# Kernel tuning notes

Measured on AMD Instinct MI355X. Metric: run time of the kernel, lower is better.

Reference implementation:

```python
import jax, jax.numpy as jnp
import numpy as np

NUM_NODES = 50000
NUM_RELS = 47        # 2*23 + 1 after enrich()
EMB_DIM = 1600
WEIGHTS_SIZE = 16
NUM_CLASSES = 50
BASES = 40
NUM_EDGES = 1600000


def setup_inputs() -> dict:
    key = jax.random.key(0)
    ks = jax.random.split(key, 8)
    return {
        "node_embeddings": jax.random.normal(ks[0], (NUM_NODES, EMB_DIM), jnp.float32),
        "comps1": jax.random.normal(ks[1], (NUM_RELS, BASES), jnp.float32),
        "bases1": jax.random.normal(ks[2], (BASES, EMB_DIM, WEIGHTS_SIZE), jnp.float32) * 0.05,
        "comps2": jax.random.normal(ks[3], (NUM_RELS, BASES), jnp.float32),
        "bases2": jax.random.normal(ks[4], (BASES, WEIGHTS_SIZE, NUM_CLASSES), jnp.float32) * 0.05,
        "bias1": jnp.zeros((WEIGHTS_SIZE,), jnp.float32),
        "bias2": jnp.zeros((NUM_CLASSES,), jnp.float32),
        "rows": jax.random.randint(ks[5], (NUM_EDGES,), 0, NUM_NODES, jnp.int32),
        "cols": jax.random.randint(ks[6], (NUM_EDGES,), 0, NUM_RELS * NUM_NODES, jnp.int32),
    }


def _spmm(rows, cols, vals, h_rel):
    # hor_graph @ h_rel : h_rel is (R*N, d); out[n] = sum_e vals[e] * h_rel[cols[e]]
    msgs = vals[:, None] * h_rel[cols]              # (E, d)
    return jax.ops.segment_sum(msgs, rows, num_segments=NUM_NODES)


def reference(node_embeddings, comps1, bases1, comps2, bases2, bias1, bias2, rows, cols):
    R, N = NUM_RELS, NUM_NODES
    # normalization: 1 / row-sums of vertical adjacency == 1 / counts per hor column
    cnt = jax.ops.segment_sum(jnp.ones_like(cols, jnp.float32), cols, num_segments=R * N)
    vals = 1.0 / cnt[cols]                          # (E,)

    # layer 1: basis-decomposed per-relation transform
    w1 = jnp.einsum('rb,bio->rio', comps1, bases1)  # (R, emb, ws)
    h = jnp.einsum('ni,rio->rno', node_embeddings, w1)  # (R, N, ws)
    h = h.reshape(R * N, WEIGHTS_SIZE)
    h = _spmm(rows, cols, vals, h)                  # (N, ws)
    h = jax.nn.relu(h + bias1)

    # layer 2
    w2 = jnp.einsum('rb,bio->rio', comps2, bases2)  # (R, ws, C)
    h = jnp.einsum('ni,rio->rno', h, w2)            # (R, N, C)
    h = h.reshape(R * N, NUM_CLASSES)
    h = _spmm(rows, cols, vals, h)                  # (N, C)
    return h + bias2
```

## Files before the change

### kernel.cpp

```cpp
#include <hip/hip_runtime.h>
#include <hip/hip_bf16.h>

#define NN 50000
#define RR 47
#define ED 1600
#define WS 16
#define NC 50
#define NB 40
#define NE 1600000
#define WJ (RR*WS)
#define WJP 768

#define GEMM_NBLK 2346
#define SCAN_B 1024
#define SCAN_NBLK ((NN + SCAN_B - 1) / SCAN_B)
#define L2ROWS 16
#define GTS 772

typedef unsigned short ushort_t;
typedef short s16x8 __attribute__((ext_vector_type(8)));
typedef short s16x4 __attribute__((ext_vector_type(4)));
typedef float f32x4 __attribute__((ext_vector_type(4)));

__device__ __forceinline__ ushort_t f2bf(float f) {
    __hip_bfloat16 h = __float2bfloat16(f);
    ushort_t u;
    __builtin_memcpy(&u, &h, 2);
    return u;
}
__device__ __forceinline__ float bf2f(ushort_t u) {
    unsigned v = ((unsigned)u) << 16;
    float f;
    __builtin_memcpy(&f, &v, 4);
    return f;
}

__device__ __forceinline__ void async_copy16(const ushort_t* g, ushort_t* l) {
    __builtin_amdgcn_global_load_lds(
        (const __attribute__((address_space(1))) unsigned int*)g,
        (__attribute__((address_space(3))) unsigned int*)l,
        16, 0, 0);
}

__global__ void cast_kernel(const float* __restrict__ X, ushort_t* __restrict__ A) {
    int idx = blockIdx.x * blockDim.x + threadIdx.x;
    if (idx >= (NN * ED) / 4) return;
    float4 v = ((const float4*)X)[idx];
    ushort_t* p = &A[idx * 4];
    p[0] = f2bf(v.x); p[1] = f2bf(v.y); p[2] = f2bf(v.z); p[3] = f2bf(v.w);
}

__global__ void count_kernel(const int* __restrict__ cols, float* __restrict__ cnt) {
    int e = blockIdx.x * blockDim.x + threadIdx.x;
    if (e < NE) atomicAdd(&cnt[cols[e]], 1.0f);
}

__global__ void wbigbt_kernel(const float* __restrict__ comps1, const float* __restrict__ bases1,
                              ushort_t* __restrict__ WbigB) {
    int idx = blockIdx.x * blockDim.x + threadIdx.x;
    if (idx >= WJP * ED) return;
    int j = idx / ED;
    int i = idx - j * ED;
    float s = 0.f;
    if (j < WJ) {
        int r = j >> 4;
        int o = j & 15;
#pragma unroll
        for (int b = 0; b < NB; ++b)
            s += comps1[r * NB + b] * bases1[(b * ED + i) * WS + o];
    }
    WbigB[idx] = f2bf(s);
}

__global__ __launch_bounds__(256) void mfma_gemm_kernel(const ushort_t* __restrict__ A,
                                                        const ushort_t* __restrict__ B,
                                                        ushort_t* __restrict__ C) {
    __shared__ ushort_t Abuf[128 * 32];
    __shared__ ushort_t Bbuf[128 * 32];

    const int bid = blockIdx.x;
    const int q = GEMM_NBLK / 8, rm = GEMM_NBLK % 8;
    const int xcd = bid & 7, loc = bid >> 3;
    const int sbid = (xcd < rm ? xcd * (q + 1) : rm * (q + 1) + (xcd - rm) * q) + loc;
    const int mb = sbid / 6;
    const int nb = sbid - mb * 6;

    const int t = threadIdx.x;
    const int lane = t & 63;
    const int wave = t >> 6;
    const int m0 = mb * 128;
    const int n0 = nb * 128;
    const int wm = (wave & 1) * 64;
    const int wn = (wave >> 1) * 64;

    const int arow0 = t >> 2,        akp0 = (t & 3) * 8;
    const int arow1 = (t + 256) >> 2, akp1 = ((t + 256) & 3) * 8;
    int gm0 = m0 + arow0; if (gm0 >= NN) gm0 = NN - 1;
    int gm1 = m0 + arow1; if (gm1 >= NN) gm1 = NN - 1;
    const ushort_t* ap0 = &A[(size_t)gm0 * ED + akp0];
    const ushort_t* ap1 = &A[(size_t)gm1 * ED + akp1];
    const ushort_t* bp0 = &B[(size_t)(n0 + arow0) * ED + akp0];
    const ushort_t* bp1 = &B[(size_t)(n0 + arow1) * ED + akp1];

    f32x4 acc[4][4];
#pragma unroll
    for (int i = 0; i < 4; ++i)
#pragma unroll
        for (int j = 0; j < 4; ++j) acc[i][j] = (f32x4){0.f, 0.f, 0.f, 0.f};

    const int frow = lane & 15;
    const int fk = (lane >> 4) * 8;

    for (int k0 = 0; k0 < ED; k0 += 32) {
        async_copy16(ap0 + k0, &Abuf[t * 8]);
        async_copy16(ap1 + k0, &Abuf[(t + 256) * 8]);
        async_copy16(bp0 + k0, &Bbuf[t * 8]);
        async_copy16(bp1 + k0, &Bbuf[(t + 256) * 8]);
        __syncthreads();

        s16x8 af[4], bf[4];
#pragma unroll
        for (int mt = 0; mt < 4; ++mt)
            af[mt] = *(const s16x8*)&Abuf[(wm + mt * 16 + frow) * 32 + fk];
#pragma unroll
        for (int nt = 0; nt < 4; ++nt)
            bf[nt] = *(const s16x8*)&Bbuf[(wn + nt * 16 + frow) * 32 + fk];
#pragma unroll
        for (int mt = 0; mt < 4; ++mt)
#pragma unroll
            for (int nt = 0; nt < 4; ++nt)
                acc[mt][nt] = __builtin_amdgcn_mfma_f32_16x16x32_bf16(af[mt], bf[nt], acc[mt][nt], 0, 0, 0);
        __syncthreads();
    }

    const int cm = (lane >> 4) * 4;
    const int cn = lane & 15;
#pragma unroll
    for (int mt = 0; mt < 4; ++mt) {
#pragma unroll
        for (int i = 0; i < 4; ++i) {
            int gm = m0 + wm + mt * 16 + cm + i;
            if (gm >= NN) continue;
#pragma unroll
            for (int nt = 0; nt < 4; ++nt) {
                int gn = n0 + wn + nt * 16 + cn;
                if (gn < WJ) C[(size_t)gm * WJ + gn] = f2bf(acc[mt][nt][i]);
            }
        }
    }
}

__global__ void hist_kernel(const int* __restrict__ rows, int* __restrict__ rcnt) {
    int e = blockIdx.x * blockDim.x + threadIdx.x;
    if (e < NE) atomicAdd(&rcnt[rows[e]], 1);
}

__global__ __launch_bounds__(SCAN_B) void scan1_kernel(const int* __restrict__ rcnt,
                                                       int* __restrict__ ptr,
                                                       int* __restrict__ bsum) {
    __shared__ int buf[2][SCAN_B];
    int t = threadIdx.x, base = blockIdx.x * SCAN_B;
    int v = (base + t < NN) ? rcnt[base + t] : 0;
    buf[0][t] = v;
    __syncthreads();
    int src = 0;
    for (int off = 1; off < SCAN_B; off <<= 1) {
        int x = buf[src][t];
        if (t >= off) x += buf[src][t - off];
        buf[src ^ 1][t] = x;
        src ^= 1;
        __syncthreads();
    }
    int incl = buf[src][t];
    if (base + t < NN) ptr[base + t] = incl - v;
    if (t == SCAN_B - 1) bsum[blockIdx.x] = incl;
}

__global__ void scan2_kernel(int* __restrict__ bsum, int* __restrict__ ptr) {
    if (threadIdx.x == 0 && blockIdx.x == 0) {
        int run = 0;
        for (int i = 0; i < SCAN_NBLK; ++i) { int v = bsum[i]; bsum[i] = run; run += v; }
        ptr[NN] = run;
    }
}

__global__ void scan3_kernel(const int* __restrict__ bsum, int* __restrict__ ptr) {
    int idx = blockIdx.x * blockDim.x + threadIdx.x;
    if (idx < NN) ptr[idx] += bsum[idx >> 10];
}

__global__ void scatter_kernel(const int* __restrict__ rows, const int* __restrict__ cols,
                               const float* __restrict__ cnt, const int* __restrict__ ptr,
                               int* __restrict__ fill, int* __restrict__ ecol,
                               float* __restrict__ eval, ushort_t* __restrict__ erow) {
    int e = blockIdx.x * blockDim.x + threadIdx.x;
    if (e >= NE) return;
    int rw = rows[e];
    int pos = ptr[rw] + atomicAdd(&fill[rw], 1);
    int c = cols[e];
    ecol[pos] = c;
    eval[pos] = 1.0f / cnt[c];
    erow[pos] = (ushort_t)rw;
}

__global__ __launch_bounds__(256) void spmm1_csr_kernel(const int* __restrict__ ptr,
        const int* __restrict__ ecol, const float* __restrict__ eval,
        const ushort_t* __restrict__ hrel, const float* __restrict__ bias1,
        float* __restrict__ h1) {
    int t = threadIdx.x;
    int wave = t >> 6, lane = t & 63;
    int m = blockIdx.x * 4 + wave;
    int start = ptr[m], end = ptr[m + 1];
    int sub = lane >> 2;
    int oq = (lane & 3) * 4;
    float acc[4] = {0.f, 0.f, 0.f, 0.f};
    for (int e0 = start; e0 < end; e0 += 16) {
        int e = e0 + sub;
        if (e < end) {
            int col = ecol[e];
            float v = eval[e];
            int r = col / NN;
            int n = col - r * NN;
            s16x4 hv = *(const s16x4*)&hrel[(size_t)n * WJ + r * WS + oq];
#pragma unroll
            for (int j = 0; j < 4; ++j)
                acc[j] += v * bf2f((ushort_t)hv[j]);
        }
    }
#pragma unroll
    for (int d = 4; d <= 32; d <<= 1)
#pragma unroll
        for (int j = 0; j < 4; ++j)
            acc[j] += __shfl_xor(acc[j], d);
    if (lane < 4) {
        float4 hv;
        float* hp = (float*)&hv;
#pragma unroll
        for (int j = 0; j < 4; ++j) {
            float x = acc[j] + bias1[oq + j];
            hp[j] = x > 0.f ? x : 0.f;
        }
        *(float4*)&h1[m * WS + oq] = hv;
    }
}

__global__ void w2pt_kernel(const float* __restrict__ comps2, const float* __restrict__ bases2,
                            ushort_t* __restrict__ w2pT) {
    int idx = blockIdx.x * blockDim.x + threadIdx.x;
    if (idx >= 64 * 768) return;
    int c = idx / 768;
    int k = idx - c * 768;
    float s = 0.f;
    if (c < NC && k < WJ) {
        int r = k >> 4;
        int o = k & 15;
#pragma unroll
        for (int b = 0; b < NB; ++b)
            s += comps2[r * NB + b] * bases2[(b * WS + o) * NC + c];
    }
    w2pT[idx] = f2bf(s);
}

__global__ __launch_bounds__(256) void layer2_kernel(const int* __restrict__ ptr,
        const int* __restrict__ ecol, const float* __restrict__ eval,
        const ushort_t* __restrict__ erow,
        const float* __restrict__ h1, const ushort_t* __restrict__ w2pT,
        const float* __restrict__ bias2, float* __restrict__ out) {
    __shared__ float gt[L2ROWS][GTS];

    int t = threadIdx.x;
    int m0 = blockIdx.x * L2ROWS;

    for (int i = t; i < L2ROWS * GTS; i += 256) ((float*)gt)[i] = 0.f;
    __syncthreads();

    {
        int estart = ptr[m0];
        int eend = ptr[m0 + L2ROWS];
        int g = t >> 4, o = t & 15;
        for (int e = estart + g; e < eend; e += 16) {
            int col = ecol[e];
            float v = eval[e];
            int lr = (int)erow[e] - m0;
            int r = col / NN;
            int n = col - r * NN;
            atomicAdd(&gt[lr][r * WS + o], v * h1[n * WS + o]);
        }
    }
    __syncthreads();

    int wave = t >> 6, lane = t & 63;
    int arow = lane & 15;
    int kx = (lane >> 4) * 8;
    int n0 = wave * 16;
    f32x4 acc = (f32x4){0.f, 0.f, 0.f, 0.f};
    const ushort_t* bbase = &w2pT[(size_t)(n0 + arow) * 768 + kx];
    for (int k0 = 0; k0 < 768; k0 += 32) {
        f32x4 a0 = *(const f32x4*)&gt[arow][k0 + kx];
        f32x4 a1 = *(const f32x4*)&gt[arow][k0 + kx + 4];
        s16x8 af;
        af[0] = (short)f2bf(a0[0]); af[1] = (short)f2bf(a0[1]);
        af[2] = (short)f2bf(a0[2]); af[3] = (short)f2bf(a0[3]);
        af[4] = (short)f2bf(a1[0]); af[5] = (short)f2bf(a1[1]);
        af[6] = (short)f2bf(a1[2]); af[7] = (short)f2bf(a1[3]);
        s16x8 bf = *(const s16x8*)&bbase[k0];
        acc = __builtin_amdgcn_mfma_f32_16x16x32_bf16(af, bf, acc, 0, 0, 0);
    }
    int cn = n0 + (lane & 15);
    if (cn < NC) {
        int rbase = (lane >> 4) * 4;
        float b2 = bias2[cn];
#pragma unroll
        for (int i = 0; i < 4; ++i) {
            int m = m0 + rbase + i;
            out[m * NC + cn] = acc[i] + b2;
        }
    }
}

extern "C" void kernel_launch(void* const* d_in, const int* in_sizes, int n_in,
                              void* d_out, int out_size, void* d_ws, size_t ws_size,
                              hipStream_t stream) {
    const float* X      = (const float*)d_in[0];
    const float* comps1 = (const float*)d_in[1];
    const float* bases1 = (const float*)d_in[2];
    const float* comps2 = (const float*)d_in[3];
    const float* bases2 = (const float*)d_in[4];
    const float* bias1  = (const float*)d_in[5];
    const float* bias2  = (const float*)d_in[6];
    const int*   rows   = (const int*)d_in[7];
    const int*   cols   = (const int*)d_in[8];
    float* out = (float*)d_out;

    char* ws = (char*)d_ws;
    float*    cnt    = (float*)   (ws + 0);
    ushort_t* Abf    = (ushort_t*)(ws + 9400064);
    int*      rowptr = (int*)     (ws + 9400064);
    int*      rcnt   = (int*)     (ws + 9600128);
    int*      fill   = (int*)     (ws + 9800192);
    int*      bsum   = (int*)     (ws + 10000256);
    int*      ecol   = (int*)     (ws + 10000512);
    float*    eval   = (float*)   (ws + 16400512);
    ushort_t* erow   = (ushort_t*)(ws + 22800512);
    ushort_t* WbigB  = (ushort_t*)(ws + 169400064);
    ushort_t* hrel   = (ushort_t*)(ws + 171857664);
    float*    h1     = (float*)   (ws + 247057664);
    ushort_t* w2pT   = (ushort_t*)(ws + 250257664);

    hipMemsetAsync(cnt, 0, (size_t)RR * NN * 4, stream);

    cast_kernel<<<(NN * ED / 4 + 255) / 256, 256, 0, stream>>>(X, Abf);
    count_kernel<<<(NE + 255) / 256, 256, 0, stream>>>(cols, cnt);
    wbigbt_kernel<<<(WJP * ED + 255) / 256, 256, 0, stream>>>(comps1, bases1, WbigB);

    mfma_gemm_kernel<<<GEMM_NBLK, 256, 0, stream>>>(Abf, WbigB, hrel);

    hipMemsetAsync(rcnt, 0, (size_t)NN * 4, stream);
    hipMemsetAsync(fill, 0, (size_t)NN * 4, stream);
    hist_kernel<<<(NE + 255) / 256, 256, 0, stream>>>(rows, rcnt);
    scan1_kernel<<<SCAN_NBLK, SCAN_B, 0, stream>>>(rcnt, rowptr, bsum);
    scan2_kernel<<<1, 64, 0, stream>>>(bsum, rowptr);
    scan3_kernel<<<(NN + 255) / 256, 256, 0, stream>>>(bsum, rowptr);
    scatter_kernel<<<(NE + 255) / 256, 256, 0, stream>>>(rows, cols, cnt, rowptr, fill, ecol, eval, erow);

    spmm1_csr_kernel<<<NN / 4, 256, 0, stream>>>(rowptr, ecol, eval, hrel, bias1, h1);

    w2pt_kernel<<<(64 * 768 + 255) / 256, 256, 0, stream>>>(comps2, bases2, w2pT);
    layer2_kernel<<<NN / L2ROWS, 256, 0, stream>>>(rowptr, ecol, eval, erow, h1, w2pT, bias2, out);
}
```

Before: 1.189 ms.

## Double-buffer GEMM LDS tiles, fuse edge histograms, widen bf16 cast stores

The GEMM main loop now uses two LDS buffers and issues the async global-to-LDS load of the next K tile before computing on the current one, dropping one barrier per iteration. The goal is to overlap memory latency with MFMA work, at the cost of twice the LDS per block. The column-count and row-histogram kernels are merged into one pass that uses integer atomics. The fp32-to-bf16 cast now converts eight elements per thread and writes them with a single 16-byte store. One risk: with one barrier per iteration, the next stage's loads could overwrite the buffer other waves are still reading unless the async copies and the barrier placement line up exactly.

```diff
diff --git a/kernel.cpp b/kernel.cpp
--- a/kernel.cpp
+++ b/kernel.cpp
@@ -44,15 +44,24 @@
 
 __global__ void cast_kernel(const float* __restrict__ X, ushort_t* __restrict__ A) {
     int idx = blockIdx.x * blockDim.x + threadIdx.x;
-    if (idx >= (NN * ED) / 4) return;
-    float4 v = ((const float4*)X)[idx];
-    ushort_t* p = &A[idx * 4];
-    p[0] = f2bf(v.x); p[1] = f2bf(v.y); p[2] = f2bf(v.z); p[3] = f2bf(v.w);
-}
-
-__global__ void count_kernel(const int* __restrict__ cols, float* __restrict__ cnt) {
+    if (idx >= (NN * ED) / 8) return;
+    const float4* xp = (const float4*)X + (size_t)idx * 2;
+    float4 a = xp[0], b = xp[1];
+    s16x8 o;
+    o[0] = (short)f2bf(a.x); o[1] = (short)f2bf(a.y);
+    o[2] = (short)f2bf(a.z); o[3] = (short)f2bf(a.w);
+    o[4] = (short)f2bf(b.x); o[5] = (short)f2bf(b.y);
+    o[6] = (short)f2bf(b.z); o[7] = (short)f2bf(b.w);
+    *(s16x8*)&A[(size_t)idx * 8] = o;
+}
+
+__global__ void edges_hist_kernel(const int* __restrict__ rows, const int* __restrict__ cols,
+                                  int* __restrict__ rcnt, int* __restrict__ ccnt) {
     int e = blockIdx.x * blockDim.x + threadIdx.x;
-    if (e < NE) atomicAdd(&cnt[cols[e]], 1.0f);
+    if (e < NE) {
+        atomicAdd(&rcnt[rows[e]], 1);
+        atomicAdd(&ccnt[cols[e]], 1);
+    }
 }
 
 __global__ void wbigbt_kernel(const float* __restrict__ comps1, const float* __restrict__ bases1,
@@ -75,8 +84,8 @@
 __global__ __launch_bounds__(256) void mfma_gemm_kernel(const ushort_t* __restrict__ A,
                                                         const ushort_t* __restrict__ B,
                                                         ushort_t* __restrict__ C) {
-    __shared__ ushort_t Abuf[128 * 32];
-    __shared__ ushort_t Bbuf[128 * 32];
+    __shared__ ushort_t Abuf[2][128 * 32];
+    __shared__ ushort_t Bbuf[2][128 * 32];
 
     const int bid = blockIdx.x;
     const int q = GEMM_NBLK / 8, rm = GEMM_NBLK % 8;
@@ -111,27 +120,34 @@
     const int frow = lane & 15;
     const int fk = (lane >> 4) * 8;
 
-    for (int k0 = 0; k0 < ED; k0 += 32) {
-        async_copy16(ap0 + k0, &Abuf[t * 8]);
-        async_copy16(ap1 + k0, &Abuf[(t + 256) * 8]);
-        async_copy16(bp0 + k0, &Bbuf[t * 8]);
-        async_copy16(bp1 + k0, &Bbuf[(t + 256) * 8]);
+#define STAGE(sel, k0) do {                              \
+        async_copy16(ap0 + (k0), &Abuf[sel][t * 8]);         \
+        async_copy16(ap1 + (k0), &Abuf[sel][(t + 256) * 8]); \
+        async_copy16(bp0 + (k0), &Bbuf[sel][t * 8]);         \
+        async_copy16(bp1 + (k0), &Bbuf[sel][(t + 256) * 8]); \
+    } while (0)
+
+    const int NT = ED / 32;
+    STAGE(0, 0);
+    for (int tt = 0; tt < NT; ++tt) {
         __syncthreads();
+        const int sel = tt & 1;
+        if (tt + 1 < NT) STAGE(sel ^ 1, (tt + 1) * 32);
 
         s16x8 af[4], bf[4];
 #pragma unroll
         for (int mt = 0; mt < 4; ++mt)
-            af[mt] = *(const s16x8*)&Abuf[(wm + mt * 16 + frow) * 32 + fk];
+            af[mt] = *(const s16x8*)&Abuf[sel][(wm + mt * 16 + frow) * 32 + fk];
 #pragma unroll
         for (int nt = 0; nt < 4; ++nt)
-            bf[nt] = *(const s16x8*)&Bbuf[(wn + nt * 16 + frow) * 32 + fk];
+            bf[nt] = *(const s16x8*)&Bbuf[sel][(wn + nt * 16 + frow) * 32 + fk];
 #pragma unroll
         for (int mt = 0; mt < 4; ++mt)
 #pragma unroll
             for (int nt = 0; nt < 4; ++nt)
                 acc[mt][nt] = __builtin_amdgcn_mfma_f32_16x16x32_bf16(af[mt], bf[nt], acc[mt][nt], 0, 0, 0);
-        __syncthreads();
-    }
+    }
+#undef STAGE
 
     const int cm = (lane >> 4) * 4;
     const int cn = lane & 15;
@@ -148,11 +164,6 @@
             }
         }
     }
-}
-
-__global__ void hist_kernel(const int* __restrict__ rows, int* __restrict__ rcnt) {
-    int e = blockIdx.x * blockDim.x + threadIdx.x;
-    if (e < NE) atomicAdd(&rcnt[rows[e]], 1);
 }
 
 __global__ __launch_bounds__(SCAN_B) void scan1_kernel(const int* __restrict__ rcnt,
@@ -190,7 +201,7 @@
 }
 
 __global__ void scatter_kernel(const int* __restrict__ rows, const int* __restrict__ cols,
-                               const float* __restrict__ cnt, const int* __restrict__ ptr,
+                               const int* __restrict__ ccnt, const int* __restrict__ ptr,
                                int* __restrict__ fill, int* __restrict__ ecol,
                                float* __restrict__ eval, ushort_t* __restrict__ erow) {
     int e = blockIdx.x * blockDim.x + threadIdx.x;
@@ -199,7 +210,7 @@
     int pos = ptr[rw] + atomicAdd(&fill[rw], 1);
     int c = cols[e];
     ecol[pos] = c;
-    eval[pos] = 1.0f / cnt[c];
+    eval[pos] = 1.0f / (float)ccnt[c];
     erow[pos] = (ushort_t)rw;
 }
 
@@ -333,7 +344,7 @@
     float* out = (float*)d_out;
 
     char* ws = (char*)d_ws;
-    float*    cnt    = (float*)   (ws + 0);
+    int*      ccnt   = (int*)     (ws + 0);
     ushort_t* Abf    = (ushort_t*)(ws + 9400064);
     int*      rowptr = (int*)     (ws + 9400064);
     int*      rcnt   = (int*)     (ws + 9600128);
@@ -347,21 +358,19 @@
     float*    h1     = (float*)   (ws + 247057664);
     ushort_t* w2pT   = (ushort_t*)(ws + 250257664);
 
-    hipMemsetAsync(cnt, 0, (size_t)RR * NN * 4, stream);
-
-    cast_kernel<<<(NN * ED / 4 + 255) / 256, 256, 0, stream>>>(X, Abf);
-    count_kernel<<<(NE + 255) / 256, 256, 0, stream>>>(cols, cnt);
+    cast_kernel<<<(NN * ED / 8 + 255) / 256, 256, 0, stream>>>(X, Abf);
     wbigbt_kernel<<<(WJP * ED + 255) / 256, 256, 0, stream>>>(comps1, bases1, WbigB);
 
     mfma_gemm_kernel<<<GEMM_NBLK, 256, 0, stream>>>(Abf, WbigB, hrel);
 
+    hipMemsetAsync(ccnt, 0, (size_t)RR * NN * 4, stream);
     hipMemsetAsync(rcnt, 0, (size_t)NN * 4, stream);
     hipMemsetAsync(fill, 0, (size_t)NN * 4, stream);
-    hist_kernel<<<(NE + 255) / 256, 256, 0, stream>>>(rows, rcnt);
+    edges_hist_kernel<<<(NE + 255) / 256, 256, 0, stream>>>(rows, cols, rcnt, ccnt);
     scan1_kernel<<<SCAN_NBLK, SCAN_B, 0, stream>>>(rcnt, rowptr, bsum);
     scan2_kernel<<<1, 64, 0, stream>>>(bsum, rowptr);
     scan3_kernel<<<(NN + 255) / 256, 256, 0, stream>>>(bsum, rowptr);
-    scatter_kernel<<<(NE + 255) / 256, 256, 0, stream>>>(rows, cols, cnt, rowptr, fill, ecol, eval, erow);
+    scatter_kernel<<<(NE + 255) / 256, 256, 0, stream>>>(rows, cols, ccnt, rowptr, fill, ecol, eval, erow);
 
     spmm1_csr_kernel<<<NN / 4, 256, 0, stream>>>(rowptr, ecol, eval, hrel, bias1, h1);
 
```

Result: no change. 1.191 ms (+0.2%).
